# Kernel tuning notes

Measured on AMD Instinct MI355X. Metric: run time of the kernel, lower is better.

Reference implementation:

```python
import jax, jax.numpy as jnp
import numpy as np

POOL = 7; SR = 2; SCALE = 1.0 / 16
NUM_CLASSES = 21
NMS_THR = 0.5; MIN_SIZE = 1.0; TOPK = 100; SCORE_THR = 0.05
BBOX_CLIP = float(np.log(1000.0 / 16))


def roi_align(feat, rois):
    # feat: [C,H,W]; rois: [P,4] xyxy in image coords. torchvision aligned=True, sampling_ratio=2.
    C, H, W = feat.shape
    S = POOL * SR
    x0r = rois[:, 0] * SCALE - 0.5
    y0r = rois[:, 1] * SCALE - 0.5
    bw = (rois[:, 2] - rois[:, 0]) * SCALE / POOL
    bh = (rois[:, 3] - rois[:, 1]) * SCALE / POOL
    t = (jnp.arange(S, dtype=feat.dtype) + 0.5) / SR  # sample offsets in bin units
    ys = y0r[:, None] + bh[:, None] * t  # [P,S]
    xs = x0r[:, None] + bw[:, None] * t  # [P,S]
    vy = (ys >= -1.0) & (ys <= H)
    vx = (xs >= -1.0) & (xs <= W)
    y = jnp.clip(ys, 0.0, H - 1)
    x = jnp.clip(xs, 0.0, W - 1)
    yl = jnp.floor(y).astype(jnp.int32); xl = jnp.floor(x).astype(jnp.int32)
    yh = jnp.minimum(yl + 1, H - 1);     xh = jnp.minimum(xl + 1, W - 1)
    ly = y - yl; lx = x - xl
    hy = 1.0 - ly; hx = 1.0 - lx

    def g(Yi, Xi):  # -> [C,P,S,S]
        return feat[:, Yi[:, :, None], Xi[:, None, :]]

    val = (g(yl, xl) * (hy[:, :, None] * hx[:, None, :])
         + g(yl, xh) * (hy[:, :, None] * lx[:, None, :])
         + g(yh, xl) * (ly[:, :, None] * hx[:, None, :])
         + g(yh, xh) * (ly[:, :, None] * lx[:, None, :]))
    val = val * (vy[:, :, None] & vx[:, None, :])[None].astype(feat.dtype)
    P = rois.shape[0]
    val = val.reshape(C, P, POOL, SR, POOL, SR).mean(axis=(3, 5))  # avg over 2x2 samples/bin
    return val.transpose(1, 0, 2, 3)  # [P,C,POOL,POOL]


def decode(pred, proposals):
    # pred: [N,K,4] (dx,dy,dw,dh); proposals: [N,4]
    w = proposals[:, 2] - proposals[:, 0]
    h = proposals[:, 3] - proposals[:, 1]
    cx = proposals[:, 0] + 0.5 * w
    cy = proposals[:, 1] + 0.5 * h
    dx, dy = pred[..., 0], pred[..., 1]
    dw = jnp.minimum(pred[..., 2], BBOX_CLIP)
    dh = jnp.minimum(pred[..., 3], BBOX_CLIP)
    pcx = dx * w[:, None] + cx[:, None]
    pcy = dy * h[:, None] + cy[:, None]
    pw = jnp.exp(dw) * w[:, None]
    ph = jnp.exp(dh) * h[:, None]
    return jnp.stack([pcx - 0.5 * pw, pcy - 0.5 * ph, pcx + 0.5 * pw, pcy + 0.5 * ph], axis=-1)


def box_iou(b):
    x1, y1, x2, y2 = b[:, 0], b[:, 1], b[:, 2], b[:, 3]
    area = (x2 - x1) * (y2 - y1)
    iw = jnp.maximum(jnp.minimum(x2[:, None], x2[None, :]) - jnp.maximum(x1[:, None], x1[None, :]), 0.0)
    ih = jnp.maximum(jnp.minimum(y2[:, None], y2[None, :]) - jnp.maximum(y1[:, None], y1[None, :]), 0.0)
    inter = iw * ih
    return inter / (area[:, None] + area[None, :] - inter)


def filter_predictions(boxes, labels, scores):
    # score threshold + min-size + per-class greedy NMS + topK, static shapes (padded to TOPK)
    N = scores.shape[0]
    ws = boxes[:, 2] - boxes[:, 0]
    hs = boxes[:, 3] - boxes[:, 1]
    valid = (scores > SCORE_THR) & (ws >= MIN_SIZE) & (hs >= MIN_SIZE)
    skey = jnp.where(valid, scores, -jnp.inf)
    order = jnp.argsort(-skey)
    b = boxes[order]; s = skey[order]; l = labels[order]; v = valid[order]
    # batched_nms via per-class coordinate offset
    off = jax.lax.stop_gradient(jnp.max(boxes) + 1.0)
    ob = jax.lax.stop_gradient(b) + (l.astype(b.dtype) * off)[:, None]
    iou = box_iou(ob)  # [N,N]
    idx = jnp.arange(N)

    def body(keep, i):
        sup = (iou[i] > NMS_THR) & keep[i] & (idx > i)
        return keep & ~sup, None

    keep, _ = jax.lax.scan(body, v, idx)
    rank = jnp.cumsum(keep) - 1
    final = keep & (rank < TOPK)
    pick = jnp.argsort(jnp.where(final, idx, N))[:TOPK]  # kept indices in score order, padded
    ok = final[pick]
    out_boxes = jnp.where(ok[:, None], b[pick], 0.0)
    out_scores = jnp.where(ok, s[pick], 0.0)
    out_labels = jnp.where(ok, l[pick], -1)
    return out_boxes, out_labels, out_scores


def roi_head_forward(image, feat, proposals, fc6_w, fc6_b, fc7_w, fc7_b, cls_w, cls_b, reg_w, reg_b):
    H_img, W_img = image.shape[-2], image.shape[-1]
    pooled = roi_align(feat[0], proposals)  # [P,C,7,7]
    x = pooled.reshape(pooled.shape[0], -1)
    x = jax.nn.relu(x @ fc6_w.T + fc6_b)
    x = jax.nn.relu(x @ fc7_w.T + fc7_b)
    cls_scores = x @ cls_w.T + cls_b                       # [P,K]
    box_pred = (x @ reg_w.T + reg_b).reshape(-1, NUM_CLASSES, 4)
    boxes = decode(box_pred, proposals)                    # [P,K,4]
    scores = jax.nn.softmax(cls_scores, axis=-1)
    boxes = jnp.stack([boxes[..., 0].clip(0, W_img), boxes[..., 1].clip(0, H_img),
                       boxes[..., 2].clip(0, W_img), boxes[..., 3].clip(0, H_img)], axis=-1)
    labels = jnp.broadcast_to(jnp.arange(NUM_CLASSES), scores.shape)
    boxes = boxes[:, 1:].reshape(-1, 4)
    scores = scores[:, 1:].reshape(-1)
    labels = (labels[:, 1:] - 1).reshape(-1)
    return filter_predictions(boxes, labels, scores)


def setup_inputs() -> dict:
    key = jax.random.key(0)
    ks = jax.random.split(key, 12)
    H_img, W_img = 800, 1072
    P, C = 300, 512
    image = jnp.zeros((1, 3, H_img, W_img), jnp.float32)
    feat = jax.random.normal(ks[0], (1, C, H_img // 16, W_img // 16), jnp.float32)
    cx = jax.random.uniform(ks[1], (P,)) * W_img
    cy = jax.random.uniform(ks[2], (P,)) * H_img
    bw = 20.0 + jax.random.uniform(ks[3], (P,)) * 300.0
    bh = 20.0 + jax.random.uniform(ks[4], (P,)) * 300.0
    proposals = jnp.stack([jnp.clip(cx - bw / 2, 0, W_img), jnp.clip(cy - bh / 2, 0, H_img),
                           jnp.clip(cx + bw / 2, 0, W_img), jnp.clip(cy + bh / 2, 0, H_img)], axis=1)
    fin = C * POOL * POOL  # 25088
    D = 1024
    fc6_w = jax.random.normal(ks[5], (D, fin), jnp.float32) / np.sqrt(fin)
    fc6_b = jnp.zeros((D,), jnp.float32)
    fc7_w = jax.random.normal(ks[6], (D, D), jnp.float32) / np.sqrt(D)
    fc7_b = jnp.zeros((D,), jnp.float32)
    cls_w = jax.random.normal(ks[7], (NUM_CLASSES, D), jnp.float32) / np.sqrt(D)
    cls_b = jnp.zeros((NUM_CLASSES,), jnp.float32)
    reg_w = jax.random.normal(ks[8], (NUM_CLASSES * 4, D), jnp.float32) * 0.001
    reg_b = jnp.zeros((NUM_CLASSES * 4,), jnp.float32)
    return {"image": image, "feat": feat, "proposals": proposals,
            "fc6_w": fc6_w, "fc6_b": fc6_b, "fc7_w": fc7_w, "fc7_b": fc7_b,
            "cls_w": cls_w, "cls_b": cls_b, "reg_w": reg_w, "reg_b": reg_b}


def reference(image, feat, proposals, fc6_w, fc6_b, fc7_w, fc7_b, cls_w, cls_b, reg_w, reg_b):
    return roi_head_forward(image, feat, proposals, fc6_w, fc6_b, fc7_w, fc7_b, cls_w, cls_b, reg_w, reg_b)
```

## Files before the change

kernel.cpp:

```cpp
#include <hip/hip_runtime.h>
#include <hip/hip_bf16.h>
#include <math.h>

#define P_N   300
#define C_N   512
#define H_F   50
#define W_F   67
#define HW_F  3350
#define D_N   1024
#define FIN   25088
#define NCLS  21
#define NCAND 6000
#define W_IMG 1072.0f
#define H_IMG 800.0f
#define BBOX_CLIP_F 4.135166556742356f
#define KS6   21
#define STEPS6_PER_Z 38
#define KS7   4
#define STEPS7_PER_Z 8
#define KSH   4
#define STEPSH_PER_Z 8
#define NHEAD 128
#define LO_SCALE 2048.0f
#define LO_INV   (1.0f/2048.0f)

typedef __attribute__((ext_vector_type(8)))  _Float16 half8;
typedef __attribute__((ext_vector_type(16))) float    f32x16;

__device__ __forceinline__ void split16(float f, _Float16& h, _Float16& l) {
  h = (_Float16)f;
  l = (_Float16)((f - (float)h) * LO_SCALE);
}

__global__ __launch_bounds__(256) void transpose_feat(const float* __restrict__ feat,
                                                      float* __restrict__ ft) {
  __shared__ float tile[32][33];
  const int s0 = blockIdx.x * 32, c0 = blockIdx.y * 32;
  const int tx = threadIdx.x, ty = threadIdx.y;
  for (int r = ty; r < 32; r += 8) {
    int c = c0 + r, s = s0 + tx;
    tile[r][tx] = (s < HW_F) ? feat[(size_t)c * HW_F + s] : 0.0f;
  }
  __syncthreads();
  for (int r = ty; r < 32; r += 8) {
    int s = s0 + r, c = c0 + tx;
    if (s < HW_F) ft[(size_t)s * C_N + c] = tile[tx][r];
  }
}

__global__ __launch_bounds__(256) void roi_align_k(const float* __restrict__ ft,
                                                   const float* __restrict__ rois,
                                                   _Float16* __restrict__ Xhi,
                                                   _Float16* __restrict__ Xlo) {
  __shared__ _Float16 hbuf[12544] __attribute__((aligned(16)));
  __shared__ _Float16 lbuf[12544] __attribute__((aligned(16)));
  __shared__ int   g_yl[14], g_yh[14], g_xl[14], g_xh[14];
  __shared__ float g_ly[14], g_hy[14], g_lx[14], g_hx[14];
  __shared__ int   g_vy[14], g_vx[14];

  const int p   = blockIdx.x;
  const int ch  = blockIdx.y;
  const int tid = threadIdx.x;

  if (tid < 14) {
    const float rx0 = rois[p*4+0], ry0 = rois[p*4+1], rx1 = rois[p*4+2], ry1 = rois[p*4+3];
    const float x0r = rx0 * 0.0625f - 0.5f;
    const float y0r = ry0 * 0.0625f - 0.5f;
    const float bw  = (rx1 - rx0) * 0.0625f * (1.0f / 7.0f);
    const float bh  = (ry1 - ry0) * 0.0625f * (1.0f / 7.0f);
    const float t   = ((float)tid + 0.5f) * 0.5f;

    const float ys = y0r + bh * t;
    g_vy[tid] = (ys >= -1.0f) && (ys <= (float)H_F);
    float y = fminf(fmaxf(ys, 0.0f), (float)(H_F - 1));
    int yi = (int)floorf(y);
    g_yl[tid] = yi; g_yh[tid] = min(yi + 1, H_F - 1);
    g_ly[tid] = y - (float)yi; g_hy[tid] = 1.0f - (y - (float)yi);

    const float xs = x0r + bw * t;
    g_vx[tid] = (xs >= -1.0f) && (xs <= (float)W_F);
    float x = fminf(fmaxf(xs, 0.0f), (float)(W_F - 1));
    int xi = (int)floorf(x);
    g_xl[tid] = xi; g_xh[tid] = min(xi + 1, W_F - 1);
    g_lx[tid] = x - (float)xi; g_hx[tid] = 1.0f - (x - (float)xi);
  }
  __syncthreads();

  const int c = ch * 256 + tid;
  for (int cell = 0; cell < 49; ++cell) {
    const int py = cell / 7;
    const int px = cell - py * 7;
    float acc = 0.0f;
#pragma unroll
    for (int sy = 0; sy < 2; ++sy) {
      const int iy = 2 * py + sy;
      if (!g_vy[iy]) continue;
      const float ly = g_ly[iy], hy = g_hy[iy];
      const int ry0i = g_yl[iy] * W_F, ry1i = g_yh[iy] * W_F;
#pragma unroll
      for (int sx = 0; sx < 2; ++sx) {
        const int ix = 2 * px + sx;
        if (!g_vx[ix]) continue;
        const float lx = g_lx[ix], hx = g_hx[ix];
        const float* b00 = ft + (size_t)(ry0i + g_xl[ix]) * C_N;
        const float* b01 = ft + (size_t)(ry0i + g_xh[ix]) * C_N;
        const float* b10 = ft + (size_t)(ry1i + g_xl[ix]) * C_N;
        const float* b11 = ft + (size_t)(ry1i + g_xh[ix]) * C_N;
        acc += (hy*hx)*b00[c] + (hy*lx)*b01[c] + (ly*hx)*b10[c] + (ly*lx)*b11[c];
      }
    }
    _Float16 h, l;
    split16(acc * 0.25f, h, l);
    hbuf[tid * 49 + cell] = h;
    lbuf[tid * 49 + cell] = l;
  }
  __syncthreads();

  const size_t base = (size_t)p * FIN + (size_t)ch * 12544;
  const uint4* hs = (const uint4*)hbuf;
  const uint4* ls = (const uint4*)lbuf;
  uint4* dh = (uint4*)(Xhi + base);
  uint4* dl = (uint4*)(Xlo + base);
  for (int k = tid; k < 1568; k += 256) { dh[k] = hs[k]; dl[k] = ls[k]; }
}

__device__ __forceinline__ int swz(int slot, int ks) {
  return slot ^ ((slot >> 5) & 1) ^ (((slot >> 3) & 1) << 1) ^ ((ks & 1) << 2);
}

__global__ __launch_bounds__(256, 2) void gemm_f16_3p(
    const _Float16* __restrict__ Ahi, const _Float16* __restrict__ Alo,
    const float* __restrict__ Wt, float* __restrict__ Pt,
    int M, int K, int steps_per_z, int ldc)
{
  __shared__ _Float16 lds[16384];
  const int tid  = threadIdx.x;
  const int lane = tid & 63, wave = tid >> 6;
  const int wm = wave >> 1, wn = wave & 1;
  const int m0 = blockIdx.x * 128, n0 = blockIdx.y * 128;
  const int steps_total = K >> 5;
  const int s0 = blockIdx.z * steps_per_z;
  const int s1 = min(s0 + steps_per_z, steps_total);

  f32x16 acc0[2][2], acc1[2][2];
#pragma unroll
  for (int a = 0; a < 2; ++a)
#pragma unroll
    for (int b = 0; b < 2; ++b) {
#pragma unroll
      for (int r = 0; r < 16; ++r) { acc0[a][b][r] = 0.f; acc1[a][b][r] = 0.f; }
    }

  const int srow = tid >> 2;
  const int j8   = tid & 3;
  const int ksW  = j8 >> 1, kc8 = j8 & 1;
  const int wslot = swz((kc8 << 5) | (srow & 31), ksW);

  for (int step = s0; step < s1; ++step) {
    const int kb = step << 5;
#pragma unroll
    for (int half = 0; half < 2; ++half) {
      const int row = srow + half * 64;
      const int mf  = row >> 5;
      const int gm  = m0 + row;
      uint4 vh = make_uint4(0,0,0,0), vl = make_uint4(0,0,0,0);
      if (gm < M) {
        vh = *reinterpret_cast<const uint4*>(Ahi + (size_t)gm * K + kb + j8 * 8);
        vl = *reinterpret_cast<const uint4*>(Alo + (size_t)gm * K + kb + j8 * 8);
      }
      const int base = (mf * 2 + ksW) * 512 + wslot * 8;
      *reinterpret_cast<uint4*>(&lds[base])        = vh;
      *reinterpret_cast<uint4*>(&lds[4096 + base]) = vl;
    }
#pragma unroll
    for (int half = 0; half < 2; ++half) {
      const int n = srow + half * 64;
      const float* wp = Wt + (size_t)(n0 + n) * K + kb + j8 * 8;
      const float4 f0 = *reinterpret_cast<const float4*>(wp);
      const float4 f1 = *reinterpret_cast<const float4*>(wp + 4);
      float fv[8] = {f0.x, f0.y, f0.z, f0.w, f1.x, f1.y, f1.z, f1.w};
      union { _Float16 h[8]; uint4 v; } uh, ul;
#pragma unroll
      for (int e = 0; e < 8; ++e) split16(fv[e], uh.h[e], ul.h[e]);
      const int nf = n >> 5;
      const int base = 8192 + (nf * 2 + ksW) * 512 + wslot * 8;
      *reinterpret_cast<uint4*>(&lds[base])        = uh.v;
      *reinterpret_cast<uint4*>(&lds[4096 + base]) = ul.v;
    }
    __syncthreads();
#pragma unroll
    for (int ks = 0; ks < 2; ++ks) {
      const int rslot = swz(lane, ks) * 8;
      half8 ah[2], al[2], bh[2], bl[2];
#pragma unroll
      for (int mi = 0; mi < 2; ++mi) {
        const int mf = wm * 2 + mi;
        ah[mi] = *reinterpret_cast<const half8*>(&lds[(mf * 2 + ks) * 512 + rslot]);
        al[mi] = *reinterpret_cast<const half8*>(&lds[4096 + (mf * 2 + ks) * 512 + rslot]);
      }
#pragma unroll
      for (int ni = 0; ni < 2; ++ni) {
        const int nf = wn * 2 + ni;
        bh[ni] = *reinterpret_cast<const half8*>(&lds[8192  + (nf * 2 + ks) * 512 + rslot]);
        bl[ni] = *reinterpret_cast<const half8*>(&lds[12288 + (nf * 2 + ks) * 512 + rslot]);
      }
#pragma unroll
      for (int mi = 0; mi < 2; ++mi)
#pragma unroll
        for (int ni = 0; ni < 2; ++ni) {
          acc0[mi][ni] = __builtin_amdgcn_mfma_f32_32x32x16_f16(ah[mi], bh[ni], acc0[mi][ni], 0, 0, 0);
          acc1[mi][ni] = __builtin_amdgcn_mfma_f32_32x32x16_f16(ah[mi], bl[ni], acc1[mi][ni], 0, 0, 0);
          acc1[mi][ni] = __builtin_amdgcn_mfma_f32_32x32x16_f16(al[mi], bh[ni], acc1[mi][ni], 0, 0, 0);
        }
    }
    __syncthreads();
  }
  const int col = lane & 31, rhi = lane >> 5;
  float* outp = Pt + (size_t)blockIdx.z * ((size_t)M * ldc);
#pragma unroll
  for (int mi = 0; mi < 2; ++mi)
#pragma unroll
    for (int ni = 0; ni < 2; ++ni) {
      const int n = n0 + (wn * 2 + ni) * 32 + col;
      if (n >= ldc) continue;
#pragma unroll
      for (int r = 0; r < 16; ++r) {
        const int m = m0 + (wm * 2 + mi) * 32 + ((r & 3) + 8 * (r >> 2) + 4 * rhi);
        if (m < M) outp[(size_t)m * ldc + n] = acc0[mi][ni][r] + acc1[mi][ni][r] * LO_INV;
      }
    }
}

__global__ __launch_bounds__(256) void reduce_bias(
    const float* __restrict__ Pt, const float* __restrict__ bias,
    float* __restrict__ out_f32, _Float16* __restrict__ out_hi, _Float16* __restrict__ out_lo,
    int MN, int KS, int nmask, int relu)
{
  int i = blockIdx.x * 256 + threadIdx.x;
  if (i >= MN) return;
  float s = 0.0f;
  for (int k = 0; k < KS; ++k) s += Pt[(size_t)k * MN + i];
  s += bias[i & nmask];
  if (relu) s = fmaxf(s, 0.0f);
  if (out_f32) out_f32[i] = s;
  if (out_hi) {
    _Float16 h, l; split16(s, h, l);
    out_hi[i] = h; out_lo[i] = l;
  }
}

__global__ __launch_bounds__(256) void prep_head(const float* __restrict__ cls_w,
                                                 const float* __restrict__ cls_b,
                                                 const float* __restrict__ reg_w,
                                                 const float* __restrict__ reg_b,
                                                 float* __restrict__ Wpad,
                                                 float* __restrict__ bpad) {
  const int row = blockIdx.x;
  const int t = threadIdx.x;
  const float* src = (row < NCLS) ? (cls_w + (size_t)row * D_N)
                   : (row < 105)  ? (reg_w + (size_t)(row - NCLS) * D_N) : nullptr;
  float4 v = make_float4(0.f, 0.f, 0.f, 0.f);
  if (src) v = reinterpret_cast<const float4*>(src)[t];
  reinterpret_cast<float4*>(Wpad + (size_t)row * D_N)[t] = v;
  if (t == 0)
    bpad[row] = (row < NCLS) ? cls_b[row] : (row < 105) ? reg_b[row - NCLS] : 0.0f;
}

__global__ __launch_bounds__(64) void decode_kernel(const float* __restrict__ logits,
                                                    const float* __restrict__ props,
                                                    float* __restrict__ cboxes,
                                                    float* __restrict__ cscores,
                                                    int* __restrict__ cvalid) {
  const int p = blockIdx.x;
  const int lane = threadIdx.x;
  const float* lg = logits + (size_t)p * NHEAD;

  float s = (lane < NCLS) ? lg[lane] : -__builtin_inff();
  float mx = s;
#pragma unroll
  for (int off = 32; off > 0; off >>= 1) mx = fmaxf(mx, __shfl_xor(mx, off));
  float e = (lane < NCLS) ? expf(s - mx) : 0.0f;
  float sum = e;
#pragma unroll
  for (int off = 32; off > 0; off >>= 1) sum += __shfl_xor(sum, off);
  const float sm = e / sum;

  if (lane >= 1 && lane < NCLS) {
    const int c = lane;
    const float x0 = props[p*4+0], y0 = props[p*4+1], x1 = props[p*4+2], y1 = props[p*4+3];
    const float w = x1 - x0, hh = y1 - y0;
    const float cx = x0 + 0.5f * w, cy = y0 + 0.5f * hh;
    const float dx = lg[NCLS + c*4 + 0];
    const float dy = lg[NCLS + c*4 + 1];
    const float dw = fminf(lg[NCLS + c*4 + 2], BBOX_CLIP_F);
    const float dh = fminf(lg[NCLS + c*4 + 3], BBOX_CLIP_F);
    const float pcx = dx * w + cx, pcy = dy * hh + cy;
    const float pw = expf(dw) * w, ph = expf(dh) * hh;
    float bx0 = pcx - 0.5f * pw, by0 = pcy - 0.5f * ph;
    float bx1 = pcx + 0.5f * pw, by1 = pcy + 0.5f * ph;
    bx0 = fminf(fmaxf(bx0, 0.0f), W_IMG);
    by0 = fminf(fmaxf(by0, 0.0f), H_IMG);
    bx1 = fminf(fmaxf(bx1, 0.0f), W_IMG);
    by1 = fminf(fmaxf(by1, 0.0f), H_IMG);
    const int idx = p * 20 + (c - 1);
    cboxes[idx*4+0] = bx0; cboxes[idx*4+1] = by0;
    cboxes[idx*4+2] = bx1; cboxes[idx*4+3] = by1;
    const bool valid = (sm > 0.05f) && ((bx1 - bx0) >= 1.0f) && ((by1 - by0) >= 1.0f);
    cscores[idx] = sm;
    cvalid[idx] = valid ? 1 : 0;
  }
}

__global__ void zero_counter(int* c) { if (threadIdx.x == 0 && blockIdx.x == 0) *c = 0; }

__global__ __launch_bounds__(256) void compact_kernel(const float* __restrict__ cscores,
                                                      const int* __restrict__ cvalid,
                                                      unsigned long long* __restrict__ ckeys,
                                                      int* __restrict__ vcount) {
  int i = blockIdx.x * 256 + threadIdx.x;
  if (i >= NCAND) return;
  if (cvalid[i]) {
    int pos = atomicAdd(vcount, 1);
    unsigned u = __float_as_uint(cscores[i]);
    ckeys[pos] = ((unsigned long long)(~u) << 32) | (unsigned)i;
  }
}

__global__ __launch_bounds__(1024) void sort_gather(const unsigned long long* __restrict__ ckeys,
                                                    const int* __restrict__ vcount,
                                                    const float* __restrict__ cboxes,
                                                    float4* __restrict__ sbox,
                                                    float* __restrict__ sscore,
                                                    int* __restrict__ slab) {
  __shared__ unsigned long long keys[8192];
  const int tid = threadIdx.x;
  const int V = *vcount;
  int Npad = 64; while (Npad < V) Npad <<= 1;
  for (int i = tid; i < Npad; i += 1024)
    keys[i] = (i < V) ? ckeys[i] : ~0ULL;
  __syncthreads();
  for (int kk = 2; kk <= Npad; kk <<= 1) {
    for (int j = kk >> 1; j > 0; j >>= 1) {
      for (int i = tid; i < Npad; i += 1024) {
        int ij = i ^ j;
        if (ij > i) {
          unsigned long long a = keys[i], b = keys[ij];
          bool up = ((i & kk) == 0);
          if ((a > b) == up) { keys[i] = b; keys[ij] = a; }
        }
      }
      __syncthreads();
    }
  }
  for (int i = tid; i < V; i += 1024) {
    unsigned long long key = keys[i];
    int idx = (int)(key & 0xffffffffu);
    sbox[i]   = *reinterpret_cast<const float4*>(&cboxes[(size_t)idx * 4]);
    sscore[i] = __uint_as_float(~(unsigned)(key >> 32));
    slab[i]   = idx % 20;
  }
}

__global__ __launch_bounds__(64) void nms_kernel(const float4* __restrict__ sbox,
                                                 const float* __restrict__ sscore,
                                                 const int* __restrict__ slab,
                                                 const int* __restrict__ vcount,
                                                 float* __restrict__ out) {
  __shared__ float4 kb[100];
  __shared__ int    kl[100];
  __shared__ float4 cb[64];
  __shared__ float  cs[64];
  __shared__ int    cl[64];
  const int lane = threadIdx.x;
  const int V = min(*vcount, NCAND);
  int nk = 0;
  for (int base = 0; base < V && nk < 100; base += 64) {
    const int i = base + lane;
    if (i < V) { cb[lane] = sbox[i]; cs[lane] = sscore[i]; cl[lane] = slab[i]; }
    __syncthreads();
    const int lim = min(64, V - base);
    for (int t = 0; t < lim; ++t) {
      if (nk >= 100) break;
      const float4 bb = cb[t];
      const int lab = cl[t];
      const float ai = (bb.z - bb.x) * (bb.w - bb.y);
      bool sup = false;
      for (int j = lane; j < nk; j += 64) {
        if (kl[j] == lab) {
          const float4 kx = kb[j];
          const float iw = fminf(kx.z, bb.z) - fmaxf(kx.x, bb.x);
          const float ih = fminf(kx.w, bb.w) - fmaxf(kx.y, bb.y);
          const float inter = fmaxf(iw, 0.0f) * fmaxf(ih, 0.0f);
          const float aj = (kx.z - kx.x) * (kx.w - kx.y);
          if (inter / (ai + aj - inter) > 0.5f) sup = true;
        }
      }
      if (!__any(sup)) {
        if (lane == 0) {
          kb[nk] = bb; kl[nk] = lab;
          out[nk*4+0] = bb.x; out[nk*4+1] = bb.y; out[nk*4+2] = bb.z; out[nk*4+3] = bb.w;
          out[400 + nk] = (float)lab;
          out[500 + nk] = cs[t];
        }
        nk++;
        __syncthreads();
      }
    }
    __syncthreads();
  }
  for (int r = nk + lane; r < 100; r += 64) {
    out[r*4+0] = 0.0f; out[r*4+1] = 0.0f; out[r*4+2] = 0.0f; out[r*4+3] = 0.0f;
    out[400 + r] = -1.0f;
    out[500 + r] = 0.0f;
  }
}

extern "C" void kernel_launch(void* const* d_in, const int* in_sizes, int n_in,
                              void* d_out, int out_size, void* d_ws, size_t ws_size,
                              hipStream_t stream) {
  const float* feat   = (const float*)d_in[1];
  const float* props  = (const float*)d_in[2];
  const float* fc6_w  = (const float*)d_in[3];
  const float* fc6_b  = (const float*)d_in[4];
  const float* fc7_w  = (const float*)d_in[5];
  const float* fc7_b  = (const float*)d_in[6];
  const float* cls_w  = (const float*)d_in[7];
  const float* cls_b  = (const float*)d_in[8];
  const float* reg_w  = (const float*)d_in[9];
  const float* reg_b  = (const float*)d_in[10];

  char* ws = (char*)d_ws;
  size_t off = 0;
  auto alloc = [&](size_t bytes) -> void* {
    void* p = ws + off;
    off += (bytes + 255) & ~(size_t)255;
    return p;
  };

  _Float16* Xhi  = (_Float16*)alloc((size_t)P_N * FIN * 2);
  _Float16* Xlo  = (_Float16*)alloc((size_t)P_N * FIN * 2);
  float*    Pt   = (float*)alloc((size_t)KS6 * P_N * D_N * 4);
  _Float16* h6hi = (_Float16*)alloc((size_t)P_N * D_N * 2);
  _Float16* h6lo = (_Float16*)alloc((size_t)P_N * D_N * 2);
  _Float16* h7hi = (_Float16*)alloc((size_t)P_N * D_N * 2);
  _Float16* h7lo = (_Float16*)alloc((size_t)P_N * D_N * 2);
  float*    Wpad = (float*)alloc((size_t)NHEAD * D_N * 4);
  float*    bpad = (float*)alloc((size_t)NHEAD * 4);
  float*  logits = (float*)alloc((size_t)P_N * NHEAD * 4);
  float*  cboxes = (float*)alloc((size_t)NCAND * 4 * 4);
  float* cscores = (float*)alloc((size_t)NCAND * 4);
  int*    cvalid = (int*)alloc((size_t)NCAND * 4);
  unsigned long long* ckeys = (unsigned long long*)alloc((size_t)NCAND * 8);
  float4*   sbox = (float4*)alloc((size_t)NCAND * 16);
  float*  sscore = (float*)alloc((size_t)NCAND * 4);
  int*      slab = (int*)alloc((size_t)NCAND * 4);
  int*    vcount = (int*)alloc(256);
  float* ft = Pt;
  (void)ws_size; (void)in_sizes; (void)n_in; (void)out_size;

  prep_head<<<NHEAD, 256, 0, stream>>>(cls_w, cls_b, reg_w, reg_b, Wpad, bpad);
  transpose_feat<<<dim3((HW_F + 31) / 32, C_N / 32), dim3(32, 8), 0, stream>>>(feat, ft);
  roi_align_k<<<dim3(P_N, 2), 256, 0, stream>>>(ft, props, Xhi, Xlo);
  gemm_f16_3p<<<dim3(3, 8, KS6), 256, 0, stream>>>(Xhi, Xlo, fc6_w, Pt, P_N, FIN, STEPS6_PER_Z, D_N);
  reduce_bias<<<(P_N * D_N + 255) / 256, 256, 0, stream>>>(
      Pt, fc6_b, nullptr, h6hi, h6lo, P_N * D_N, KS6, D_N - 1, 1);
  gemm_f16_3p<<<dim3(3, 8, KS7), 256, 0, stream>>>(h6hi, h6lo, fc7_w, Pt, P_N, D_N, STEPS7_PER_Z, D_N);
  reduce_bias<<<(P_N * D_N + 255) / 256, 256, 0, stream>>>(
      Pt, fc7_b, nullptr, h7hi, h7lo, P_N * D_N, KS7, D_N - 1, 1);
  gemm_f16_3p<<<dim3(3, 1, KSH), 256, 0, stream>>>(h7hi, h7lo, Wpad, Pt, P_N, D_N, STEPSH_PER_Z, NHEAD);
  reduce_bias<<<(P_N * NHEAD + 255) / 256, 256, 0, stream>>>(
      Pt, bpad, logits, nullptr, nullptr, P_N * NHEAD, KSH, NHEAD - 1, 0);
  decode_kernel<<<P_N, 64, 0, stream>>>(logits, props, cboxes, cscores, cvalid);
  zero_counter<<<1, 1, 0, stream>>>(vcount);
  compact_kernel<<<(NCAND + 255) / 256, 256, 0, stream>>>(cscores, cvalid, ckeys, vcount);
  sort_gather<<<1, 1024, 0, stream>>>(ckeys, vcount, cboxes, sbox, sscore, slab);
  nms_kernel<<<1, 64, 0, stream>>>(sbox, sscore, slab, vcount, (float*)d_out);
}
```

Before: 343.6 us.

## Parallelize NMS with bitmask IoU matrix, deepen split-K, remap GEMM blocks

Replaces the serial single-wave greedy NMS with a parallel kernel that computes a pairwise same-class suppression bitmask over all sorted candidates, followed by a single-wave scan that walks live bits and applies mask rows. Separately, it doubles or quadruples the split-K factors for the fc6, fc7 and head GEMMs to launch more blocks, and remaps flat block ids across groups of eight, likely to spread work across XCDs. The risks are extra partial-sum traffic in reduce_bias, an O(V^2) mask computation with a 4.6MB buffer, and an NMS scan that still iterates serially over candidates.

Measured after the change: 344.9 us. No clear change (+0.4%).

```diff
diff --git a/kernel.cpp b/kernel.cpp
--- a/kernel.cpp
+++ b/kernel.cpp
@@ -14,13 +14,14 @@
 #define W_IMG 1072.0f
 #define H_IMG 800.0f
 #define BBOX_CLIP_F 4.135166556742356f
-#define KS6   21
-#define STEPS6_PER_Z 38
-#define KS7   4
-#define STEPS7_PER_Z 8
-#define KSH   4
-#define STEPSH_PER_Z 8
+#define KS6   42
+#define STEPS6_PER_Z 19
+#define KS7   16
+#define STEPS7_PER_Z 2
+#define KSH   16
+#define STEPSH_PER_Z 2
 #define NHEAD 128
+#define NW    96
 #define LO_SCALE 2048.0f
 #define LO_INV   (1.0f/2048.0f)
 
@@ -137,9 +138,18 @@
   const int tid  = threadIdx.x;
   const int lane = tid & 63, wave = tid >> 6;
   const int wm = wave >> 1, wn = wave & 1;
-  const int m0 = blockIdx.x * 128, n0 = blockIdx.y * 128;
+
+  const int GX = gridDim.x, GY = gridDim.y;
+  const int T  = GX * GY * gridDim.z;
+  int flat = blockIdx.x + GX * (blockIdx.y + GY * blockIdx.z);
+  if ((T & 7) == 0) flat = (flat & 7) * (T >> 3) + (flat >> 3);
+  const int bx = flat % GX;
+  const int by = (flat / GX) % GY;
+  const int bz = flat / (GX * GY);
+
+  const int m0 = bx * 128, n0 = by * 128;
   const int steps_total = K >> 5;
-  const int s0 = blockIdx.z * steps_per_z;
+  const int s0 = bz * steps_per_z;
   const int s1 = min(s0 + steps_per_z, steps_total);
 
   f32x16 acc0[2][2], acc1[2][2];
@@ -216,7 +226,7 @@
     __syncthreads();
   }
   const int col = lane & 31, rhi = lane >> 5;
-  float* outp = Pt + (size_t)blockIdx.z * ((size_t)M * ldc);
+  float* outp = Pt + (size_t)bz * ((size_t)M * ldc);
 #pragma unroll
   for (int mi = 0; mi < 2; ++mi)
 #pragma unroll
@@ -361,52 +371,64 @@
   }
 }
 
-__global__ __launch_bounds__(64) void nms_kernel(const float4* __restrict__ sbox,
-                                                 const float* __restrict__ sscore,
-                                                 const int* __restrict__ slab,
-                                                 const int* __restrict__ vcount,
-                                                 float* __restrict__ out) {
-  __shared__ float4 kb[100];
-  __shared__ int    kl[100];
-  __shared__ float4 cb[64];
-  __shared__ float  cs[64];
-  __shared__ int    cl[64];
+__global__ __launch_bounds__(256) void iou_matrix(const float4* __restrict__ sbox,
+                                                  const int* __restrict__ slab,
+                                                  const int* __restrict__ vcount,
+                                                  unsigned long long* __restrict__ mask) {
+  const int V = *vcount;
+  const int i = blockIdx.x * 4 + (threadIdx.x >> 6);
+  const int lane = threadIdx.x & 63;
+  if (i >= V) return;
+  const float4 bi = sbox[i];
+  const int li = slab[i];
+  const float ai = (bi.z - bi.x) * (bi.w - bi.y);
+  const int nw = (V + 63) >> 6;
+  for (int w = 0; w < nw; ++w) {
+    const int j = (w << 6) + lane;
+    bool sup = false;
+    if (j > i && j < V && slab[j] == li) {
+      const float4 bj = sbox[j];
+      const float iw = fminf(bi.z, bj.z) - fmaxf(bi.x, bj.x);
+      const float ih = fminf(bi.w, bj.w) - fmaxf(bi.y, bj.y);
+      const float inter = fmaxf(iw, 0.0f) * fmaxf(ih, 0.0f);
+      const float aj = (bj.z - bj.x) * (bj.w - bj.y);
+      sup = inter / (ai + aj - inter) > 0.5f;
+    }
+    const unsigned long long m = __ballot(sup);
+    if (lane == 0) mask[(size_t)i * NW + w] = m;
+  }
+}
+
+__global__ __launch_bounds__(64) void nms_scan(const float4* __restrict__ sbox,
+                                               const float* __restrict__ sscore,
+                                               const int* __restrict__ slab,
+                                               const int* __restrict__ vcount,
+                                               const unsigned long long* __restrict__ mask,
+                                               float* __restrict__ out) {
   const int lane = threadIdx.x;
   const int V = min(*vcount, NCAND);
+  unsigned long long live0 = ~0ULL, live1 = ~0ULL;
   int nk = 0;
-  for (int base = 0; base < V && nk < 100; base += 64) {
-    const int i = base + lane;
-    if (i < V) { cb[lane] = sbox[i]; cs[lane] = sscore[i]; cl[lane] = slab[i]; }
-    __syncthreads();
-    const int lim = min(64, V - base);
-    for (int t = 0; t < lim; ++t) {
-      if (nk >= 100) break;
-      const float4 bb = cb[t];
-      const int lab = cl[t];
-      const float ai = (bb.z - bb.x) * (bb.w - bb.y);
-      bool sup = false;
-      for (int j = lane; j < nk; j += 64) {
-        if (kl[j] == lab) {
-          const float4 kx = kb[j];
-          const float iw = fminf(kx.z, bb.z) - fmaxf(kx.x, bb.x);
-          const float ih = fminf(kx.w, bb.w) - fmaxf(kx.y, bb.y);
-          const float inter = fmaxf(iw, 0.0f) * fmaxf(ih, 0.0f);
-          const float aj = (kx.z - kx.x) * (kx.w - kx.y);
-          if (inter / (ai + aj - inter) > 0.5f) sup = true;
-        }
-      }
-      if (!__any(sup)) {
-        if (lane == 0) {
-          kb[nk] = bb; kl[nk] = lab;
-          out[nk*4+0] = bb.x; out[nk*4+1] = bb.y; out[nk*4+2] = bb.z; out[nk*4+3] = bb.w;
-          out[400 + nk] = (float)lab;
-          out[500 + nk] = cs[t];
-        }
-        nk++;
-        __syncthreads();
-      }
-    }
-    __syncthreads();
+  for (int i = 0; i < V && nk < 100; ++i) {
+    const int wi = i >> 6, bi = i & 63;
+    union { unsigned long long u; uint2 v; } t;
+    t.u = (wi < 64) ? live0 : live1;
+    const int src = (wi < 64) ? wi : (wi - 64);
+    const unsigned lo = __shfl(t.v.x, src);
+    const unsigned hi = __shfl(t.v.y, src);
+    const unsigned long long wv = ((unsigned long long)hi << 32) | lo;
+    if ((wv >> bi) & 1ULL) {
+      if (lane == 0) {
+        const float4 bb = sbox[i];
+        out[nk*4+0] = bb.x; out[nk*4+1] = bb.y; out[nk*4+2] = bb.z; out[nk*4+3] = bb.w;
+        out[400 + nk] = (float)slab[i];
+        out[500 + nk] = sscore[i];
+      }
+      const unsigned long long* mrow = mask + (size_t)i * NW;
+      live0 &= ~mrow[lane];
+      if (lane < NW - 64) live1 &= ~mrow[64 + lane];
+      nk++;
+    }
   }
   for (int r = nk + lane; r < 100; r += 64) {
     out[r*4+0] = 0.0f; out[r*4+1] = 0.0f; out[r*4+2] = 0.0f; out[r*4+3] = 0.0f;
@@ -454,6 +476,7 @@
   float4*   sbox = (float4*)alloc((size_t)NCAND * 16);
   float*  sscore = (float*)alloc((size_t)NCAND * 4);
   int*      slab = (int*)alloc((size_t)NCAND * 4);
+  unsigned long long* supmask = (unsigned long long*)alloc((size_t)NCAND * NW * 8);
   int*    vcount = (int*)alloc(256);
   float* ft = Pt;
   (void)ws_size; (void)in_sizes; (void)n_in; (void)out_size;
@@ -474,5 +497,6 @@
   zero_counter<<<1, 1, 0, stream>>>(vcount);
   compact_kernel<<<(NCAND + 255) / 256, 256, 0, stream>>>(cscores, cvalid, ckeys, vcount);
   sort_gather<<<1, 1024, 0, stream>>>(ckeys, vcount, cboxes, sbox, sscore, slab);
-  nms_kernel<<<1, 64, 0, stream>>>(sbox, sscore, slab, vcount, (float*)d_out);
-}
+  iou_matrix<<<(NCAND + 3) / 4, 256, 0, stream>>>(sbox, slab, vcount, supmask);
+  nms_scan<<<1, 64, 0, stream>>>(sbox, sscore, slab, vcount, supmask, (float*)d_out);
+}
```
